# Optimization experiments

Measured on AMD Instinct MI355X. Metric: run time of the kernel, lower is better.

The kernel has to match this reference:

```python
import jax, jax.numpy as jnp
import numpy as np
from math import factorial

# ---- configuration (init_kwargs: nclasses=40, cfg.bw=16) ----
BW = 16            # spherical bandwidth
NB = 2 * BW        # grid samples per angle
M = 2 * BW - 1     # spectral orders m in [-(BW-1), BW-1]
OFF = BW - 1       # index offset: m -> m + OFF
NCLS = 40
EPS = 1e-5
BATCH = 8

_FACT = [float(factorial(i)) for i in range(4 * BW + 2)]

def _wigner_d(l, beta):
    """Wigner small-d matrix d^l_{m',m}(beta), shape [2l+1, 2l+1]."""
    c, s = np.cos(beta / 2.0), np.sin(beta / 2.0)
    d = np.zeros((2 * l + 1, 2 * l + 1))
    for imp, mp in enumerate(range(-l, l + 1)):
        for im, m in enumerate(range(-l, l + 1)):
            pref = np.sqrt(_FACT[l + mp] * _FACT[l - mp] * _FACT[l + m] * _FACT[l - m])
            acc = 0.0
            for k in range(max(0, m - mp), min(l + m, l - mp) + 1):
                acc += ((-1.0) ** (mp - m + k)
                        / (_FACT[l + m - k] * _FACT[k] * _FACT[l - k - mp] * _FACT[k - m + mp])
                        * c ** (2 * l - 2 * k + m - mp) * s ** (2 * k - m + mp))
            d[imp, im] = pref * acc
    return d

def _build_constants():
    # Driscoll-Healy beta quadrature grid and weights
    betas = np.pi * (2 * np.arange(NB) + 1) / (4 * BW)
    kk = np.arange(BW)
    qw = (2.0 / BW) * np.sin(betas) * (
        np.sin(np.outer(2 * np.arange(NB) + 1, 2 * kk + 1) * np.pi / (4 * BW)) @ (1.0 / (2 * kk + 1)))
    d_beta = np.zeros((NB, BW, M, M))      # d^l_{mn}(beta_j), zero-padded over l
    for j, beta in enumerate(betas):
        for l in range(BW):
            d_beta[j, l, OFF - l:OFF + l + 1, OFF - l:OFF + l + 1] = _wigner_d(l, beta)
    d_eq = np.zeros((BW, M, M))            # d^l_{mn}(pi/2) for the equatorial kernel grid
    for l in range(BW):
        d_eq[l, OFF - l:OFF + l + 1, OFF - l:OFF + l + 1] = _wigner_d(l, np.pi / 2)
    bins = (np.arange(-(BW - 1), BW) % NB).astype(np.int32)  # FFT bin for each order m
    return qw.astype(np.float32), d_beta.astype(np.float32), d_eq.astype(np.float32), bins

_QWn, _DBETAn, _DEQn, _BINSn = _build_constants()
_DBJ = jnp.asarray(_DBETAn)                                   # [NB, L, M, M]
_DEQJ = jnp.asarray(_DEQn)                                    # [L, M, M]
_DEQ0 = jnp.asarray(_DEQn[:, :, OFF])                         # [L, M]  (n = 0 column)
_WD_S2 = jnp.asarray(_QWn[:, None, None] * _DBETAn[:, :, :, OFF])   # [NB, L, M]
_WD_SO3 = jnp.asarray(_QWn[:, None, None, None] * _DBETAn)          # [NB, L, M, M]
_L2 = jnp.asarray((2.0 * np.arange(BW) + 1.0).astype(np.float32))
_BINSJ = jnp.asarray(_BINSn)

def _so3_ifft(z, bias):
    # z: [B, Co, L, M, M] SO(3) spectrum -> real signal [B, Co, NB(beta), NB(alpha), NB(gamma)]
    F = jnp.einsum('bolmn,jlmn,l->bojmn', z, _DBJ, _L2)
    grid = jnp.zeros(F.shape[:3] + (NB, NB), F.dtype)
    grid = grid.at[..., _BINSJ[:, None], _BINSJ[None, :]].set(F)
    sig = jnp.fft.ifft2(grid, axes=(-2, -1)).real * float(NB * NB)
    return sig + bias[None, :, None, None, None]

def _s2_conv(x, W, bias):
    # x: [B, Ci, NB(beta), NB(alpha)]; W: [Ci, Co, NB] kernel on the equatorial grid
    Xf = jnp.fft.fft(x, axis=-1)[..., _BINSJ]                 # [B,Ci,NB,M]
    xh = jnp.einsum('bcjm,jlm->bclm', Xf, _WD_S2)             # S2 FFT -> [B,Ci,L,M]
    Wf = jnp.fft.fft(W, axis=-1)[..., _BINSJ]                 # [Ci,Co,M]
    yh = _DEQ0[:, :, None, None] * jnp.transpose(Wf, (2, 0, 1))[None]   # [L,N,Ci,Co]
    z = jnp.einsum('bilm,lnio->bolmn', xh, jnp.conj(yh))      # S2 correlation -> SO(3) spectrum
    return _so3_ifft(z, bias)

def _so3_conv(x, W, bias):
    # x: [B, Ci, NB(beta), NB(alpha), NB(gamma)]; W: [Ci, Co, NB]
    Xf = jnp.fft.fft2(x, axes=(-2, -1))[..., _BINSJ[:, None], _BINSJ[None, :]]  # [B,Ci,NB,M,M]
    xh = jnp.einsum('bcjmn,jlmn->bclmn', Xf, _WD_SO3)         # SO(3) FFT -> [B,Ci,L,M,M]
    Wf = jnp.fft.fft(W, axis=-1)[..., _BINSJ]                 # [Ci,Co,M]
    yh = _DEQJ[:, :, :, None, None] * jnp.transpose(Wf, (2, 0, 1))[None, :, None]  # [L,N,K,Ci,Co]
    z = jnp.einsum('bilmk,lnkio->bolmn', xh, jnp.conj(yh))    # SO(3) correlation
    return _so3_ifft(z, bias)

def _bn(h, g, b, axes, shape):
    mu = jnp.mean(h, axes, keepdims=True)
    var = jnp.var(h, axes, keepdims=True)
    return (h - mu) * jax.lax.rsqrt(var + EPS) * g.reshape(shape) + b.reshape(shape)

def _forward(x, k1, c1b, bn1_g, bn1_b, k2, c2b, bn2_g, bn2_b, k3, c3b, bn3_g, bn3_b,
             fc1_w, fc1_b, fbn1_g, fbn1_b, fc2_w, fc2_b, fbn2_g, fbn2_b, fc3_w, fc3_b):
    s5 = (1, -1, 1, 1, 1)
    h = _s2_conv(x, k1, c1b)                                  # [B,50,NB,NB,NB]
    h = jax.nn.relu(_bn(h, bn1_g, bn1_b, (0, 2, 3, 4), s5))
    h = _so3_conv(h, k2, c2b)
    h = jax.nn.relu(_bn(h, bn2_g, bn2_b, (0, 2, 3, 4), s5))
    h = _so3_conv(h, k3, c3b)
    h = jax.nn.relu(_bn(h, bn3_g, bn3_b, (0, 2, 3, 4), s5))
    h = h.mean(-1)                                            # integrate over gamma
    h = h.reshape(h.shape[0], h.shape[1], -1).max(-1)         # global max pool -> [B,50]
    h = h @ fc1_w.T + fc1_b
    h = jax.nn.relu(_bn(h, fbn1_g, fbn1_b, (0,), (1, -1)))
    h = h @ fc2_w.T + fc2_b
    h = jax.nn.relu(_bn(h, fbn2_g, fbn2_b, (0,), (1, -1)))
    h = h @ fc3_w.T + fc3_b
    return jax.nn.log_softmax(h, axis=1)

def setup_inputs():
    key = jax.random.key(0)
    ks = jax.random.split(key, 24)
    f32 = jnp.float32
    def kern(k, ci, co):
        return jax.random.normal(k, (ci, co, NB), f32) / np.sqrt(ci * NB).astype(np.float32)
    def lin(k, co, ci):
        return jax.random.normal(k, (co, ci), f32) / np.sqrt(ci).astype(np.float32)
    return {
        'x': jax.random.normal(ks[0], (BATCH, 1, NB, NB), f32),
        'k1': kern(ks[1], 1, 50), 'c1b': 0.01 * jax.random.normal(ks[2], (50,), f32),
        'bn1_g': 1.0 + 0.1 * jax.random.normal(ks[3], (50,), f32),
        'bn1_b': 0.1 * jax.random.normal(ks[4], (50,), f32),
        'k2': kern(ks[5], 50, 50), 'c2b': 0.01 * jax.random.normal(ks[6], (50,), f32),
        'bn2_g': 1.0 + 0.1 * jax.random.normal(ks[7], (50,), f32),
        'bn2_b': 0.1 * jax.random.normal(ks[8], (50,), f32),
        'k3': kern(ks[9], 50, 50), 'c3b': 0.01 * jax.random.normal(ks[10], (50,), f32),
        'bn3_g': 1.0 + 0.1 * jax.random.normal(ks[11], (50,), f32),
        'bn3_b': 0.1 * jax.random.normal(ks[12], (50,), f32),
        'fc1_w': lin(ks[13], 256, 50), 'fc1_b': jnp.zeros((256,), f32),
        'fbn1_g': 1.0 + 0.1 * jax.random.normal(ks[14], (256,), f32),
        'fbn1_b': 0.1 * jax.random.normal(ks[15], (256,), f32),
        'fc2_w': lin(ks[16], 128, 256), 'fc2_b': jnp.zeros((128,), f32),
        'fbn2_g': 1.0 + 0.1 * jax.random.normal(ks[17], (128,), f32),
        'fbn2_b': 0.1 * jax.random.normal(ks[18], (128,), f32),
        'fc3_w': lin(ks[19], NCLS, 128), 'fc3_b': jnp.zeros((NCLS,), f32),
    }

def reference(x, k1, c1b, bn1_g, bn1_b, k2, c2b, bn2_g, bn2_b, k3, c3b, bn3_g, bn3_b,
              fc1_w, fc1_b, fbn1_g, fbn1_b, fc2_w, fc2_b, fbn2_g, fbn2_b, fc3_w, fc3_b):
    return _forward(x, k1, c1b, bn1_g, bn1_b, k2, c2b, bn2_g, bn2_b, k3, c3b, bn3_g, bn3_b,
                    fc1_w, fc1_b, fbn1_g, fbn1_b, fc2_w, fc2_b, fbn2_g, fbn2_b, fc3_w, fc3_b)
```

## Files before the change

kernel.cpp:

```cpp
#include <hip/hip_runtime.h>
#include <math.h>

constexpr int NB = 32;
constexpr int LL = 16;
constexpr int MM = 31;
constexpr int MOFF = 15;
constexpr int NBATCH = 8;
constexpr int NCH = 50;
constexpr int NQ = MM * MM;
constexpr int SPAT = NB * NB * NB;
constexpr long long HN = (long long)NBATCH * NCH * SPAT;

#define PI_D 3.14159265358979323846

__device__ inline float2 c_mk(float x, float y) { float2 r; r.x = x; r.y = y; return r; }

__device__ inline void fill_tw(float2* tw) {
  int t = threadIdx.x;
  if (t < 32) {
    double a = (double)t * (PI_D / 16.0);
    tw[t] = c_mk((float)cos(a), (float)sin(a));
  }
}

__device__ inline int bitrev5(int n) {
  return ((n & 1) << 4) | ((n & 2) << 2) | (n & 4) | ((n & 8) >> 2) | ((n & 16) >> 4);
}

__device__ inline double dpow(double x, int n) {
  double r = 1.0;
  for (int i = 0; i < n; ++i) r *= x;
  return r;
}


__global__ void qw_kernel(float* __restrict__ qw) {
  int j = threadIdx.x;
  if (j >= NB) return;
  double beta = PI_D * (2 * j + 1) / 64.0;
  double acc = 0.0;
  for (int kk = 0; kk < LL; ++kk)
    acc += sin((double)(2 * j + 1) * (2 * kk + 1) * PI_D / 64.0) / (double)(2 * kk + 1);
  qw[j] = (float)((2.0 / 16.0) * sin(beta) * acc);
}

__global__ void wigner_kernel(float* __restrict__ out, int nj, int eqmode) {
  __shared__ double fact[66];
  int tid = threadIdx.x;
  if (tid < 66) { double f = 1.0; for (int i = 2; i <= tid; ++i) f *= (double)i; fact[tid] = f; }
  __syncthreads();
  int total = nj * LL * NQ;
  int idx = blockIdx.x * blockDim.x + tid;
  if (idx >= total) return;
  int q = idx % NQ;
  int l = (idx / NQ) % LL;
  int j = idx / (NQ * LL);
  int mp = q / MM - MOFF;
  int m  = q % MM - MOFF;
  int amp = mp < 0 ? -mp : mp, am = m < 0 ? -m : m;
  float res = 0.f;
  if (amp <= l && am <= l) {
    double beta = eqmode ? (PI_D * 0.5) : (PI_D * (2 * j + 1) / 64.0);
    double c = cos(beta * 0.5), s = sin(beta * 0.5);
    double pref = sqrt(fact[l + mp] * fact[l - mp] * fact[l + m] * fact[l - m]);
    int k0 = max(0, m - mp), k1 = min(l + m, l - mp);
    double acc = 0.0;
    for (int k = k0; k <= k1; ++k) {
      double denom = fact[l + m - k] * fact[k] * fact[l - k - mp] * fact[k - m + mp];
      double term = dpow(c, 2 * l - 2 * k + m - mp) * dpow(s, 2 * k - m + mp) / denom;
      acc += ((mp - m + k) & 1) ? -term : term;
    }
    res = (float)(pref * acc);
  }
  out[idx] = res;
}

__global__ void transpose_d_kernel(const float* __restrict__ dbeta, float* __restrict__ dbT) {
  int idx = blockIdx.x * blockDim.x + threadIdx.x;
  if (idx >= NB * LL * NQ) return;
  int m = idx % MM;
  int n = (idx / MM) % MM;
  int jl = idx / NQ;
  dbT[idx] = dbeta[jl * NQ + m * MM + n];
}

__global__ void make_dbl_kernel(const float* __restrict__ dbeta, const float* __restrict__ qw,
                                float* __restrict__ dbl) {
  int idx = blockIdx.x * blockDim.x + threadIdx.x;
  if (idx >= NB * NQ * LL) return;
  int l = idx % LL;
  int q = (idx / LL) % NQ;
  int j = idx / (LL * NQ);
  dbl[idx] = qw[j] * dbeta[(j * LL + l) * NQ + q];
}


__global__ __launch_bounds__(256) void s2_xh_kernel(const float* __restrict__ x,
                                                    const float* __restrict__ qw,
                                                    const float* __restrict__ dbeta,
                                                    float2* __restrict__ xh1) {
  __shared__ float xt[NB * NB];
  __shared__ float2 Xf0[NB * MM];
  __shared__ float2 tw[32];
  fill_tw(tw);
  int tid = threadIdx.x, b = blockIdx.x;
  for (int e = tid; e < NB * NB; e += 256) xt[e] = x[b * 1024 + e];
  __syncthreads();
  for (int e = tid; e < NB * MM; e += 256) {
    int j = e / MM, mi = e % MM, m = mi - MOFF;
    float re = 0.f, im = 0.f;
    const float* row = xt + j * NB;
    for (int a = 0; a < NB; ++a) {
      float v = row[a];
      float2 t = tw[(m * a) & 31];
      re += v * t.x; im -= v * t.y;
    }
    Xf0[e] = c_mk(re, im);
  }
  __syncthreads();
  for (int e = tid; e < LL * MM; e += 256) {
    int l = e / MM, mi = e % MM;
    float re = 0.f, im = 0.f;
    for (int j = 0; j < NB; ++j) {
      float w = qw[j] * dbeta[(j * LL + l) * NQ + mi * MM + MOFF];
      float2 X = Xf0[j * MM + mi];
      re += w * X.x; im += w * X.y;
    }
    xh1[(b * LL + l) * MM + mi] = c_mk(re, im);
  }
}

__global__ __launch_bounds__(256) void wfft_kernel(const float* __restrict__ W, int CiCo,
                                                   float2* __restrict__ Wf) {
  __shared__ float2 tw[32];
  fill_tw(tw);
  __syncthreads();
  int idx = blockIdx.x * blockDim.x + threadIdx.x;
  if (idx >= MM * CiCo) return;
  int ni = idx / CiCo, ic = idx % CiCo;
  int n = ni - MOFF;
  float re = 0.f, im = 0.f;
  for (int t = 0; t < NB; ++t) {
    float v = W[ic * NB + t];
    float2 tt = tw[(n * t) & 31];
    re += v * tt.x; im -= v * tt.y;
  }
  Wf[idx] = c_mk(re, im);
}

__global__ void s2_z_kernel(const float2* __restrict__ xh1, const float2* __restrict__ Wf1,
                            const float* __restrict__ deq, float2* __restrict__ z) {
  int idx = blockIdx.x * blockDim.x + threadIdx.x;
  if (idx >= NBATCH * NCH * LL * NQ) return;
  int mi = idx % MM; int t = idx / MM;
  int ni = t % MM; t /= MM;
  int l = t % LL; t /= LL;
  int o = t % NCH; int b = t / NCH;
  float d0 = deq[(l * MM + ni) * MM + MOFF];
  float2 xv = xh1[(b * LL + l) * MM + mi];
  float2 wv = Wf1[ni * NCH + o];
  float re = d0 * (xv.x * wv.x + xv.y * wv.y);
  float im = d0 * (xv.y * wv.x - xv.x * wv.y);
  z[idx] = c_mk(re, im);
}


__global__ __launch_bounds__(256) void fjq_kernel(const float2* __restrict__ z,
                                                  const float* __restrict__ dbT,
                                                  float2* __restrict__ F) {
  __shared__ float2 zs[2][LL][8];
  int qg = blockIdx.x % 121;
  int bg = blockIdx.x / 121;
  int tid = threadIdx.x;
  int j = tid >> 3, ql = tid & 7;
  int q = qg * 8 + ql;
  bool qok = q < NQ;
  int qc = qok ? q : NQ - 1;
  float w[LL];
  #pragma unroll
  for (int l = 0; l < LL; ++l)
    w[l] = (2.f * l + 1.f) * dbT[(j * LL + l) * NQ + qc];
  int bo0 = bg * 25;
  if (tid < 128) {
    int l = tid >> 3, qq = qg * 8 + (tid & 7);
    int dd = (qq < NQ) ? (qq / MM - MOFF) : 99; if (dd < 0) dd = -dd;
    zs[0][l][tid & 7] = (l >= dd) ? z[((long long)bo0 * LL + l) * NQ + qq] : c_mk(0.f, 0.f);
  }
  __syncthreads();
  for (int i = 0; i < 25; ++i) {
    int bo = bo0 + i;
    if (i < 24 && tid < 128) {
      int l = tid >> 3, qq = qg * 8 + (tid & 7);
      int dd = (qq < NQ) ? (qq / MM - MOFF) : 99; if (dd < 0) dd = -dd;
      zs[(i + 1) & 1][l][tid & 7] =
          (l >= dd) ? z[((long long)(bo + 1) * LL + l) * NQ + qq] : c_mk(0.f, 0.f);
    }
    float fr = 0.f, fi = 0.f;
    #pragma unroll
    for (int l = 0; l < LL; ++l) {
      float2 zv = zs[i & 1][l][ql];
      fr += w[l] * zv.x; fi += w[l] * zv.y;
    }
    if (qok) F[((long long)bo * NB + j) * NQ + q] = c_mk(fr, fi);
    __syncthreads();
  }
}

__global__ __launch_bounds__(64) void so3_dft_kernel(const float2* __restrict__ F,
                                                     const float* __restrict__ bias,
                                                     float* __restrict__ out,
                                                     float2* __restrict__ parts) {
  __shared__ float S[2][32][33];
  __shared__ float2 tw[32];
  fill_tw(tw);
  int tid = threadIdx.x;
  int lane = tid & 31;
  int t = tid >> 5;
  int idx = blockIdx.x * 2 + t;
  int j = idx & 31;
  int bo = idx >> 5;
  int o = bo % NCH;
  __syncthreads();

  float vr[32], vi[32];

  int mi = (lane + 15) & 31;
  const float2* src = F + ((long long)bo * NB + j) * NQ + mi;
  bool mok = mi < MM;
  #pragma unroll
  for (int kn = 0; kn < 32; ++kn) {
    const int ni = (kn + 15) & 31;
    if (ni < MM) {
      float2 v = mok ? src[ni * MM] : c_mk(0.f, 0.f);
      vr[kn] = v.x; vi[kn] = v.y;
    } else { vr[kn] = 0.f; vi[kn] = 0.f; }
  }

  #pragma unroll
  for (int st = 0; st < 5; ++st) {
    const int half = 16 >> st, tmul = 1 << st;
    #pragma unroll
    for (int p = 0; p < 16; ++p) {
      const int j2 = p & (half - 1);
      const int i0 = ((p >> (4 - st)) << (5 - st)) + j2;
      const int i1 = i0 + half;
      float2 tt = tw[(j2 * tmul) & 31];
      float ur = vr[i0], ui = vi[i0], wr = vr[i1], wi = vi[i1];
      float dr = ur - wr, di = ui - wi;
      vr[i0] = ur + wr; vi[i0] = ui + wi;
      vr[i1] = dr * tt.x - di * tt.y;
      vi[i1] = dr * tt.y + di * tt.x;
    }
  }

  #pragma unroll
  for (int g = 0; g < 32; ++g) S[t][g][lane] = vr[bitrev5(g)];
  __syncthreads();
  #pragma unroll
  for (int k = 0; k < 32; ++k) vr[k] = S[t][lane][k];
  __syncthreads();
  #pragma unroll
  for (int g = 0; g < 32; ++g) S[t][g][lane] = vi[bitrev5(g)];
  __syncthreads();
  #pragma unroll
  for (int k = 0; k < 32; ++k) vi[k] = S[t][lane][k];

  #pragma unroll
  for (int st = 0; st < 5; ++st) {
    const int half = 16 >> st, tmul = 1 << st;
    #pragma unroll
    for (int p = 0; p < 16; ++p) {
      const int j2 = p & (half - 1);
      const int i0 = ((p >> (4 - st)) << (5 - st)) + j2;
      const int i1 = i0 + half;
      float2 tt = tw[(j2 * tmul) & 31];
      float ur = vr[i0], ui = vi[i0], wr = vr[i1], wi = vi[i1];
      float dr = ur - wr, di = ui - wi;
      vr[i0] = ur + wr; vi[i0] = ui + wi;
      vr[i1] = dr * tt.x - di * tt.y;
      vi[i1] = dr * tt.y + di * tt.x;
    }
  }

  float bval = bias[o];
  long long obase = (long long)bo * SPAT + (long long)j * 1024 + lane;
  float s1 = 0.f, s2 = 0.f;
  #pragma unroll
  for (int a = 0; a < 32; ++a) {
    float val = vr[bitrev5(a)] + bval;
    out[obase + a * 32] = val;
    s1 += val; s2 += val * val;
  }
  #pragma unroll
  for (int off = 32; off > 0; off >>= 1) {
    s1 += __shfl_down(s1, off);
    s2 += __shfl_down(s2, off);
  }
  if (tid == 0) {
    atomicAdd(&parts[bo].x, s1);
    atomicAdd(&parts[bo].y, s2);
  }
}


__global__ void bn_finalize_kernel(const float2* __restrict__ partials,
                                   const float* __restrict__ g, const float* __restrict__ bb,
                                   float2* __restrict__ sc) {
  int o = threadIdx.x;
  if (o >= NCH) return;
  float s = 0.f, ss = 0.f;
  for (int b = 0; b < NBATCH; ++b) { float2 p = partials[b * NCH + o]; s += p.x; ss += p.y; }
  float inv = 1.f / (float)(NBATCH * SPAT);
  float mu = s * inv;
  float var = ss * inv - mu * mu;
  float scale = g[o] * rsqrtf(var + 1e-5f);
  sc[o] = c_mk(scale, bb[o] - mu * scale);
}


__global__ __launch_bounds__(64) void dft2f_kernel(const float* __restrict__ h,
                                                   const float2* __restrict__ sc,
                                                   float2* __restrict__ Xf) {
  __shared__ float S[2][32][33];
  __shared__ float2 tw[32];
  fill_tw(tw);
  int tid = threadIdx.x;
  int lane = tid & 31;
  int t = tid >> 5;
  long long idx = blockIdx.x * 2 + t;
  int c = (int)((idx >> 5) % NCH);
  float2 s = sc[c];
  __syncthreads();

  float vr[32], vi[32];

  const float4* hp = reinterpret_cast<const float4*>(h + idx * 1024 + lane * 32);
  #pragma unroll
  for (int q4 = 0; q4 < 8; ++q4) {
    float4 v = hp[q4];
    vr[q4 * 4 + 0] = fmaxf(v.x * s.x + s.y, 0.f);
    vr[q4 * 4 + 1] = fmaxf(v.y * s.x + s.y, 0.f);
    vr[q4 * 4 + 2] = fmaxf(v.z * s.x + s.y, 0.f);
    vr[q4 * 4 + 3] = fmaxf(v.w * s.x + s.y, 0.f);
    vi[q4 * 4 + 0] = 0.f; vi[q4 * 4 + 1] = 0.f;
    vi[q4 * 4 + 2] = 0.f; vi[q4 * 4 + 3] = 0.f;
  }

  #pragma unroll
  for (int st = 0; st < 5; ++st) {
    const int half = 16 >> st, tmul = 1 << st;
    #pragma unroll
    for (int p = 0; p < 16; ++p) {
      const int j2 = p & (half - 1);
      const int i0 = ((p >> (4 - st)) << (5 - st)) + j2;
      const int i1 = i0 + half;
      float2 tt = tw[(j2 * tmul) & 31];
      float ur = vr[i0], ui = vi[i0], wr = vr[i1], wi = vi[i1];
      float dr = ur - wr, di = ui - wi;
      vr[i0] = ur + wr; vi[i0] = ui + wi;
      vr[i1] = dr * tt.x + di * tt.y;
      vi[i1] = di * tt.x - dr * tt.y;
    }
  }

  #pragma unroll
  for (int k = 0; k < 32; ++k) S[t][k][lane] = vr[bitrev5(k)];
  __syncthreads();
  #pragma unroll
  for (int a = 0; a < 32; ++a) vr[a] = S[t][lane][a];
  __syncthreads();
  #pragma unroll
  for (int k = 0; k < 32; ++k) S[t][k][lane] = vi[bitrev5(k)];
  __syncthreads();
  #pragma unroll
  for (int a = 0; a < 32; ++a) vi[a] = S[t][lane][a];

  #pragma unroll
  for (int st = 0; st < 5; ++st) {
    const int half = 16 >> st, tmul = 1 << st;
    #pragma unroll
    for (int p = 0; p < 16; ++p) {
      const int j2 = p & (half - 1);
      const int i0 = ((p >> (4 - st)) << (5 - st)) + j2;
      const int i1 = i0 + half;
      float2 tt = tw[(j2 * tmul) & 31];
      float ur = vr[i0], ui = vi[i0], wr = vr[i1], wi = vi[i1];
      float dr = ur - wr, di = ui - wi;
      vr[i0] = ur + wr; vi[i0] = ui + wi;
      vr[i1] = dr * tt.x + di * tt.y;
      vi[i1] = di * tt.x - dr * tt.y;
    }
  }

  int ni = (lane + 15) & 31;
  if (ni < MM) {
    float2* dst = Xf + idx * NQ + ni;
    #pragma unroll
    for (int mi = 0; mi < MM; ++mi) {
      const int km = (mi + 17) & 31;
      dst[mi * MM] = c_mk(vr[bitrev5(km)], vi[bitrev5(km)]);
    }
  }
}

__global__ void xh_kernel(const float2* __restrict__ Xf, const float* __restrict__ dbl,
                          float2* __restrict__ xh) {
  int idx = blockIdx.x * blockDim.x + threadIdx.x;
  if (idx >= NBATCH * NCH * NQ) return;
  int q = idx % NQ;
  int bc = idx / NQ;
  int dm = q / MM - MOFF; if (dm < 0) dm = -dm;
  int dn = q % MM - MOFF; if (dn < 0) dn = -dn;
  int lmin = dm > dn ? dm : dn;
  float2 acc[LL];
  #pragma unroll
  for (int l = 0; l < LL; ++l) acc[l] = c_mk(0.f, 0.f);
  const float4* dbase = reinterpret_cast<const float4*>(dbl) + (long long)q * 4;
  const float2* xbase = Xf + (long long)bc * NB * NQ + q;
  for (int j = 0; j < NB; ++j) {
    float2 xv = xbase[(long long)j * NQ];
    const float4* d4 = dbase + (long long)j * NQ * 4;
    float4 w0 = d4[0], w1 = d4[1], w2 = d4[2], w3 = d4[3];
    float wv[16] = {w0.x, w0.y, w0.z, w0.w, w1.x, w1.y, w1.z, w1.w,
                    w2.x, w2.y, w2.z, w2.w, w3.x, w3.y, w3.z, w3.w};
    #pragma unroll
    for (int l = 0; l < LL; ++l) {
      acc[l].x += wv[l] * xv.x;
      acc[l].y += wv[l] * xv.y;
    }
  }
  #pragma unroll
  for (int l = 0; l < LL; ++l)
    if (l >= lmin) xh[((long long)bc * LL + l) * NQ + q] = acc[l];
}

__global__ __launch_bounds__(64) void hk_kernel(const float2* __restrict__ xh,
                                                const float* __restrict__ deq,
                                                float2* __restrict__ hk2) {
  int r = blockIdx.x;
  int mi = r % MM;
  int lb = r / MM;
  int b = lb & 7;
  int l = lb >> 3;
  int adm = mi - MOFF; adm = adm < 0 ? -adm : adm;
  if (adm > l) return;
  int ich = threadIdx.x;
  if (ich >= NCH) return;
  float2 row[MM];
  const float2* src = xh + ((long long)(b * NCH + ich) * LL + l) * NQ + mi * MM;
  #pragma unroll
  for (int k = 0; k < MM; ++k) row[k] = src[k];
  const float* dl = deq + l * NQ;
  long long obase = (long long)r * MM * NCH + ich;
  for (int ni = MOFF - l; ni <= MOFF + l; ++ni) {
    const float* dr = dl + ni * MM;
    float re = 0.f, im = 0.f;
    #pragma unroll
    for (int k = 0; k < MM; ++k) {
      float d = dr[k];
      re += d * row[k].x;
      im += d * row[k].y;
    }
    hk2[obase + (long long)ni * NCH] = c_mk(re, im);
  }
}

__global__ __launch_bounds__(256) void z_kernel(const float2* __restrict__ hk2,
                                                const float2* __restrict__ Wf,
                                                float2* __restrict__ z) {
  __shared__ float2 ws[NCH * NCH];
  int blk = blockIdx.x;
  int ni = 0;
  for (;;) {
    int d = ni - MOFF; if (d < 0) d = -d;
    int nt = 32 - 2 * d;
    if (blk < nt) break;
    blk -= nt; ++ni;
  }
  int dmin = ni - MOFF; if (dmin < 0) dmin = -dmin;
  int tid = threadIdx.x;
  {
    const float4* s4 = reinterpret_cast<const float4*>(Wf + ni * (NCH * NCH));
    float4* d4 = reinterpret_cast<float4*>(ws);
    for (int e = tid; e < NCH * NCH / 2; e += 256) d4[e] = s4[e];
  }
  __syncthreads();
  if (tid >= 248) return;
  int r = dmin * 248 + blk * 124 + (tid % 124);
  int o0 = (tid / 124) * 25;
  int mi = r % MM;
  int rem = r / MM;
  int b = rem & 7;
  int l = rem >> 3;

  const float4* h4 = reinterpret_cast<const float4*>(hk2 + ((long long)r * MM + ni) * NCH);

  float2 acc[25];
  #pragma unroll
  for (int u = 0; u < 25; ++u) acc[u] = c_mk(0.f, 0.f);

  for (int ih = 0; ih < 25; ++ih) {
    float4 hv = h4[ih];
    const float2* w0 = ws + (2 * ih) * NCH + o0;
    #pragma unroll
    for (int u = 0; u < 25; ++u) {
      float2 w = w0[u];
      acc[u].x += hv.x * w.x + hv.y * w.y;
      acc[u].y += hv.y * w.x - hv.x * w.y;
    }
    const float2* w1 = w0 + NCH;
    #pragma unroll
    for (int u = 0; u < 25; ++u) {
      float2 w = w1[u];
      acc[u].x += hv.z * w.x + hv.w * w.y;
      acc[u].y += hv.w * w.x - hv.z * w.y;
    }
  }

  long long zbase = (((long long)(b * NCH + o0) * LL + l) * NQ) + ni * MM + mi;
  #pragma unroll
  for (int u = 0; u < 25; ++u)
    z[zbase + (long long)u * LL * NQ] = acc[u];
}


__global__ void pool_kernel(const float* __restrict__ h, const float2* __restrict__ sc,
                            float* __restrict__ pooled) {
  __shared__ float sm[256];
  int tid = threadIdx.x;
  int o = blockIdx.x % NCH;
  float2 s = sc[o];
  const float* base = h + (long long)blockIdx.x * SPAT;
  float best = -1e30f;
  for (int e = tid; e < 1024; e += 256) {
    float acc = 0.f;
    for (int g = 0; g < NB; ++g) {
      float v = base[e * NB + g];
      acc += fmaxf(v * s.x + s.y, 0.f);
    }
    best = fmaxf(best, acc * (1.f / 32.f));
  }
  sm[tid] = best;
  __syncthreads();
  for (int st = 128; st > 0; st >>= 1) {
    if (tid < st) sm[tid] = fmaxf(sm[tid], sm[tid + st]);
    __syncthreads();
  }
  if (tid == 0) pooled[blockIdx.x] = sm[0];
}

__global__ __launch_bounds__(32) void fc1_kernel(const float* __restrict__ pooled,
    const float* __restrict__ fc1w, const float* __restrict__ fc1b,
    const float* __restrict__ g1, const float* __restrict__ b1,
    float* __restrict__ A) {
  int o = blockIdx.x * 32 + threadIdx.x;
  const float* wr = fc1w + o * NCH;
  float v[NBATCH];
  float bias = fc1b[o];
  #pragma unroll
  for (int b = 0; b < NBATCH; ++b) v[b] = bias;
  for (int c = 0; c < NCH; ++c) {
    float w = wr[c];
    #pragma unroll
    for (int b = 0; b < NBATCH; ++b) v[b] += pooled[b * NCH + c] * w;
  }
  float s = 0.f, ss = 0.f;
  #pragma unroll
  for (int b = 0; b < NBATCH; ++b) { s += v[b]; ss += v[b] * v[b]; }
  float mu = s * 0.125f, var = ss * 0.125f - mu * mu;
  float scl = g1[o] * rsqrtf(var + 1e-5f), sh = b1[o] - mu * scl;
  #pragma unroll
  for (int b = 0; b < NBATCH; ++b) A[b * 256 + o] = fmaxf(v[b] * scl + sh, 0.f);
}

__global__ __launch_bounds__(64) void fc2_kernel(const float* __restrict__ A,
    const float* __restrict__ fc2w, const float* __restrict__ fc2b,
    const float* __restrict__ g2, const float* __restrict__ b2,
    float* __restrict__ A2) {
  int tid = threadIdx.x;
  int o = blockIdx.x * 8 + (tid >> 3);
  int b = tid & 7;
  const float4* av = reinterpret_cast<const float4*>(A + b * 256);
  const float4* wv = reinterpret_cast<const float4*>(fc2w + o * 256);
  float acc = fc2b[o];
  #pragma unroll
  for (int c4 = 0; c4 < 64; ++c4) {
    float4 a = av[c4], w = wv[c4];
    acc += a.x * w.x + a.y * w.y + a.z * w.z + a.w * w.w;
  }
  float s = acc, ss = acc * acc;
  #pragma unroll
  for (int m = 1; m < 8; m <<= 1) {
    s += __shfl_xor(s, m);
    ss += __shfl_xor(ss, m);
  }
  float mu = s * 0.125f, var = ss * 0.125f - mu * mu;
  float scl = g2[o] * rsqrtf(var + 1e-5f), sh = b2[o] - mu * scl;
  A2[b * 128 + o] = fmaxf(acc * scl + sh, 0.f);
}

__global__ __launch_bounds__(64) void fc3_kernel(const float* __restrict__ A2,
    const float* __restrict__ fc3w, const float* __restrict__ fc3b,
    float* __restrict__ out) {
  __shared__ float Cm[40];
  int tid = threadIdx.x;
  int b = blockIdx.x;
  if (tid < 40) {
    const float* wr = fc3w + tid * 128;
    const float* ar = A2 + b * 128;
    float acc = fc3b[tid];
    #pragma unroll
    for (int c = 0; c < 128; ++c) acc += ar[c] * wr[c];
    Cm[tid] = acc;
  }
  __syncthreads();
  if (tid == 0) {
    float mx = -1e30f;
    for (int f = 0; f < 40; ++f) mx = fmaxf(mx, Cm[f]);
    float se = 0.f;
    for (int f = 0; f < 40; ++f) se += expf(Cm[f] - mx);
    float lse = mx + logf(se);
    for (int f = 0; f < 40; ++f) out[b * 40 + f] = Cm[f] - lse;
  }
}


extern "C" void kernel_launch(void* const* d_in, const int* in_sizes, int n_in,
                              void* d_out, int out_size, void* d_ws, size_t ws_size,
                              hipStream_t stream) {
  (void)in_sizes; (void)n_in; (void)out_size;
  const float* x    = (const float*)d_in[0];
  const float* k1   = (const float*)d_in[1];
  const float* c1b  = (const float*)d_in[2];
  const float* bn1g = (const float*)d_in[3];
  const float* bn1b = (const float*)d_in[4];
  const float* k2   = (const float*)d_in[5];
  const float* c2b  = (const float*)d_in[6];
  const float* bn2g = (const float*)d_in[7];
  const float* bn2b = (const float*)d_in[8];
  const float* k3   = (const float*)d_in[9];
  const float* c3b  = (const float*)d_in[10];
  const float* bn3g = (const float*)d_in[11];
  const float* bn3b = (const float*)d_in[12];
  const float* fc1w = (const float*)d_in[13];
  const float* fc1b = (const float*)d_in[14];
  const float* g1   = (const float*)d_in[15];
  const float* bb1  = (const float*)d_in[16];
  const float* fc2w = (const float*)d_in[17];
  const float* fc2b = (const float*)d_in[18];
  const float* g2   = (const float*)d_in[19];
  const float* bb2  = (const float*)d_in[20];
  const float* fc3w = (const float*)d_in[21];
  const float* fc3b = (const float*)d_in[22];
  float* out = (float*)d_out;

  char* ws = (char*)d_ws;
  size_t off = 0;
  auto alloc = [&](size_t n) -> char* {
    char* p = ws + off;
    off += (n + 255) & ~(size_t)255;
    return p;
  };

  float*  dbeta  = (float*)alloc(sizeof(float) * NB * LL * NQ);
  float*  dbT    = (float*)alloc(sizeof(float) * NB * LL * NQ);
  float*  dbl    = (float*)alloc(sizeof(float) * NB * NQ * LL);
  float*  deq    = (float*)alloc(sizeof(float) * LL * NQ);
  float*  qw     = (float*)alloc(sizeof(float) * NB);
  float2* xh1    = (float2*)alloc(sizeof(float2) * NBATCH * LL * MM);
  float2* Wf     = (float2*)alloc(sizeof(float2) * MM * NCH * NCH);
  float2* parts  = (float2*)alloc(sizeof(float2) * NBATCH * NCH);
  float2* bnsc   = (float2*)alloc(sizeof(float2) * 64);
  float*  pooled = (float*)alloc(sizeof(float) * NBATCH * NCH);
  float*  Abuf   = (float*)alloc(sizeof(float) * NBATCH * 256);
  float*  A2buf  = (float*)alloc(sizeof(float) * NBATCH * 128);
  float*  HA     = (float*)alloc(sizeof(float) * (size_t)HN);
  float*  HB     = (float*)alloc(sizeof(float) * (size_t)HN);
  size_t XFB = (size_t)NBATCH * NCH * NB * NQ * sizeof(float2);
  size_t XHB = (size_t)NBATCH * NCH * LL * NQ * sizeof(float2);
  char* AR = alloc(XFB + XHB);
  float2* Xf  = (float2*)AR;
  float2* xh  = (float2*)(AR + XFB);
  float2* hk2 = (float2*)AR;
  float2* zb  = (float2*)(AR + XFB);
  float2* Fb  = (float2*)AR;

  if (ws_size < off) return;

  const int T = 256;
  const size_t PARTS_B = sizeof(float2) * NBATCH * NCH;
  qw_kernel<<<1, 32, 0, stream>>>(qw);
  wigner_kernel<<<(NB * LL * NQ + T - 1) / T, T, 0, stream>>>(dbeta, NB, 0);
  wigner_kernel<<<(LL * NQ + T - 1) / T, T, 0, stream>>>(deq, 1, 1);
  transpose_d_kernel<<<(NB * LL * NQ + T - 1) / T, T, 0, stream>>>(dbeta, dbT);
  make_dbl_kernel<<<(NB * NQ * LL + T - 1) / T, T, 0, stream>>>(dbeta, qw, dbl);

  s2_xh_kernel<<<NBATCH, T, 0, stream>>>(x, qw, dbeta, xh1);
  wfft_kernel<<<(MM * 1 * NCH + T - 1) / T, T, 0, stream>>>(k1, 1 * NCH, Wf);
  s2_z_kernel<<<(NBATCH * NCH * LL * NQ + T - 1) / T, T, 0, stream>>>(xh1, Wf, deq, zb);
  fjq_kernel<<<121 * 16, T, 0, stream>>>(zb, dbT, Fb);
  hipMemsetAsync(parts, 0, PARTS_B, stream);
  so3_dft_kernel<<<NBATCH * NCH * NB / 2, 64, 0, stream>>>(Fb, c1b, HA, parts);
  bn_finalize_kernel<<<1, 64, 0, stream>>>(parts, bn1g, bn1b, bnsc);

  dft2f_kernel<<<NBATCH * NCH * NB / 2, 64, 0, stream>>>(HA, bnsc, Xf);
  xh_kernel<<<(NBATCH * NCH * NQ + T - 1) / T, T, 0, stream>>>(Xf, dbl, xh);
  wfft_kernel<<<(MM * NCH * NCH + T - 1) / T, T, 0, stream>>>(k2, NCH * NCH, Wf);
  hk_kernel<<<NBATCH * LL * MM, 64, 0, stream>>>(xh, deq, hk2);
  z_kernel<<<512, T, 0, stream>>>(hk2, Wf, zb);
  fjq_kernel<<<121 * 16, T, 0, stream>>>(zb, dbT, Fb);
  hipMemsetAsync(parts, 0, PARTS_B, stream);
  so3_dft_kernel<<<NBATCH * NCH * NB / 2, 64, 0, stream>>>(Fb, c2b, HB, parts);
  bn_finalize_kernel<<<1, 64, 0, stream>>>(parts, bn2g, bn2b, bnsc);

  dft2f_kernel<<<NBATCH * NCH * NB / 2, 64, 0, stream>>>(HB, bnsc, Xf);
  xh_kernel<<<(NBATCH * NCH * NQ + T - 1) / T, T, 0, stream>>>(Xf, dbl, xh);
  wfft_kernel<<<(MM * NCH * NCH + T - 1) / T, T, 0, stream>>>(k3, NCH * NCH, Wf);
  hk_kernel<<<NBATCH * LL * MM, 64, 0, stream>>>(xh, deq, hk2);
  z_kernel<<<512, T, 0, stream>>>(hk2, Wf, zb);
  fjq_kernel<<<121 * 16, T, 0, stream>>>(zb, dbT, Fb);
  hipMemsetAsync(parts, 0, PARTS_B, stream);
  so3_dft_kernel<<<NBATCH * NCH * NB / 2, 64, 0, stream>>>(Fb, c3b, HA, parts);
  bn_finalize_kernel<<<1, 64, 0, stream>>>(parts, bn3g, bn3b, bnsc);

  pool_kernel<<<NBATCH * NCH, T, 0, stream>>>(HA, bnsc, pooled);
  fc1_kernel<<<8, 32, 0, stream>>>(pooled, fc1w, fc1b, g1, bb1, Abuf);
  fc2_kernel<<<16, 64, 0, stream>>>(Abuf, fc2w, fc2b, g2, bb2, A2buf);
  fc3_kernel<<<8, 64, 0, stream>>>(A2buf, fc3w, fc3b, out);
}
```

Before: 689.5 us.

## Tile xh_kernel over q and batch-channels, staging Wigner weights in shared memory

xh_kernel is reorganised so that each 256-thread block covers 16 q positions for 16 batch-channel rows. The block loads the matching dbl weight tile (32 beta samples by 16 l values by 16 q) into LDS once and shares it across all 16 rows. Previously every thread read its own weights from global memory. This cuts redundant global weight traffic, at the cost of partially wasted work in the last q tile and poorer coalescing of Xf loads, since only 16 q values are contiguous per row.

```diff
diff --git a/kernel.cpp b/kernel.cpp
--- a/kernel.cpp
+++ b/kernel.cpp
@@ -403,24 +403,49 @@
   }
 }
 
-__global__ void xh_kernel(const float2* __restrict__ Xf, const float* __restrict__ dbl,
-                          float2* __restrict__ xh) {
-  int idx = blockIdx.x * blockDim.x + threadIdx.x;
-  if (idx >= NBATCH * NCH * NQ) return;
-  int q = idx % NQ;
-  int bc = idx / NQ;
+__global__ __launch_bounds__(256) void xh_kernel(const float2* __restrict__ Xf,
+                                                 const float* __restrict__ dbl,
+                                                 float2* __restrict__ xh) {
+  __shared__ __align__(16) float4 dblS[NB * 4 * 16];
+  int tile = blockIdx.x % 61;
+  int grp  = blockIdx.x / 61;
+  int tid = threadIdx.x;
+  int ql = tid & 15;
+  int bl = tid >> 4;
+  int q0 = tile * 16;
+  int q = q0 + ql;
+  bool qok = q < NQ;
+  int bc = grp * 16 + bl;
+
+  {
+    const float4* src = reinterpret_cast<const float4*>(dbl);
+    #pragma unroll
+    for (int k = 0; k < 8; ++k) {
+      int e = k * 256 + tid;
+      int l4 = e & 3;
+      int qq = (e >> 2) & 15;
+      int j = e >> 6;
+      int qg = q0 + qq; if (qg >= NQ) qg = NQ - 1;
+      dblS[(j * 4 + l4) * 16 + qq] = src[((long long)j * NQ + qg) * 4 + l4];
+    }
+  }
+  __syncthreads();
+
   int dm = q / MM - MOFF; if (dm < 0) dm = -dm;
   int dn = q % MM - MOFF; if (dn < 0) dn = -dn;
   int lmin = dm > dn ? dm : dn;
+
   float2 acc[LL];
   #pragma unroll
   for (int l = 0; l < LL; ++l) acc[l] = c_mk(0.f, 0.f);
-  const float4* dbase = reinterpret_cast<const float4*>(dbl) + (long long)q * 4;
+
   const float2* xbase = Xf + (long long)bc * NB * NQ + q;
   for (int j = 0; j < NB; ++j) {
-    float2 xv = xbase[(long long)j * NQ];
-    const float4* d4 = dbase + (long long)j * NQ * 4;
-    float4 w0 = d4[0], w1 = d4[1], w2 = d4[2], w3 = d4[3];
+    float2 xv = qok ? xbase[(long long)j * NQ] : c_mk(0.f, 0.f);
+    float4 w0 = dblS[(j * 4 + 0) * 16 + ql];
+    float4 w1 = dblS[(j * 4 + 1) * 16 + ql];
+    float4 w2 = dblS[(j * 4 + 2) * 16 + ql];
+    float4 w3 = dblS[(j * 4 + 3) * 16 + ql];
     float wv[16] = {w0.x, w0.y, w0.z, w0.w, w1.x, w1.y, w1.z, w1.w,
                     w2.x, w2.y, w2.z, w2.w, w3.x, w3.y, w3.z, w3.w};
     #pragma unroll
@@ -429,9 +454,11 @@
       acc[l].y += wv[l] * xv.y;
     }
   }
-  #pragma unroll
-  for (int l = 0; l < LL; ++l)
-    if (l >= lmin) xh[((long long)bc * LL + l) * NQ + q] = acc[l];
+  if (qok) {
+    #pragma unroll
+    for (int l = 0; l < LL; ++l)
+      if (l >= lmin) xh[((long long)bc * LL + l) * NQ + q] = acc[l];
+  }
 }
 
 __global__ __launch_bounds__(64) void hk_kernel(const float2* __restrict__ xh,
@@ -704,7 +731,7 @@
   bn_finalize_kernel<<<1, 64, 0, stream>>>(parts, bn1g, bn1b, bnsc);
 
   dft2f_kernel<<<NBATCH * NCH * NB / 2, 64, 0, stream>>>(HA, bnsc, Xf);
-  xh_kernel<<<(NBATCH * NCH * NQ + T - 1) / T, T, 0, stream>>>(Xf, dbl, xh);
+  xh_kernel<<<61 * 25, T, 0, stream>>>(Xf, dbl, xh);
   wfft_kernel<<<(MM * NCH * NCH + T - 1) / T, T, 0, stream>>>(k2, NCH * NCH, Wf);
   hk_kernel<<<NBATCH * LL * MM, 64, 0, stream>>>(xh, deq, hk2);
   z_kernel<<<512, T, 0, stream>>>(hk2, Wf, zb);
@@ -714,7 +741,7 @@
   bn_finalize_kernel<<<1, 64, 0, stream>>>(parts, bn2g, bn2b, bnsc);
 
   dft2f_kernel<<<NBATCH * NCH * NB / 2, 64, 0, stream>>>(HB, bnsc, Xf);
-  xh_kernel<<<(NBATCH * NCH * NQ + T - 1) / T, T, 0, stream>>>(Xf, dbl, xh);
+  xh_kernel<<<61 * 25, T, 0, stream>>>(Xf, dbl, xh);
   wfft_kernel<<<(MM * NCH * NCH + T - 1) / T, T, 0, stream>>>(k3, NCH * NCH, Wf);
   hk_kernel<<<NBATCH * LL * MM, 64, 0, stream>>>(xh, deq, hk2);
   z_kernel<<<512, T, 0, stream>>>(hk2, Wf, zb);
```

Measured after the change: 849.9 us. 1.23x slower.
